# Kernel optimization log

Measured on AMD Instinct MI355X. Metric: run time of the kernel, lower is better.

## Reference

```python
import jax, jax.numpy as jnp
import numpy as np

IN_F, OUT_F, K = 1024, 1024, 12
EPS = 1e-6


def setup_inputs() -> dict:
    key = jax.random.key(0)
    k1, k2, k3, k4 = jax.random.split(key, 4)
    x = jax.random.normal(k1, (4, 4096, IN_F), dtype=jnp.float32)
    # grid: linspace(-2,2,K) per feature + small noise so sort is nontrivial
    base = jnp.linspace(-2.0, 2.0, K, dtype=jnp.float32)
    grid = base[None, :] + 0.1 * jax.random.normal(k2, (IN_F, K), dtype=jnp.float32)
    coeffs = 0.1 * jax.random.normal(k3, (IN_F, K), dtype=jnp.float32)
    tangents = jnp.zeros((IN_F, K), dtype=jnp.float32)
    knot_alive = jnp.full((IN_F, K), 3.0, dtype=jnp.float32)
    kw1, kw2 = jax.random.split(k4)
    proj_w = jax.random.normal(kw1, (OUT_F, IN_F), dtype=jnp.float32) / np.sqrt(IN_F)
    proj_b = jnp.zeros((OUT_F,), dtype=jnp.float32)
    res_w = jax.random.normal(kw2, (OUT_F, IN_F), dtype=jnp.float32) / np.sqrt(IN_F)
    return {"x": x, "grid": grid, "coeffs": coeffs, "tangents": tangents,
            "knot_alive": knot_alive, "proj_w": proj_w, "proj_b": proj_b, "res_w": res_w}


def _eval_hermite_spline(x, grid, coeffs, tangents, knot_alive):
    # sort knots per input feature (grid: [F,K])
    sort_idx = jnp.argsort(grid, axis=1)
    sorted_grid = jnp.take_along_axis(grid, sort_idx, axis=1)
    sorted_coeffs = jnp.take_along_axis(coeffs, sort_idx, axis=1)
    sorted_tangents = jnp.take_along_axis(tangents, sort_idx, axis=1)
    sorted_alive = jnp.take_along_axis(knot_alive, sort_idx, axis=1)
    alive = jax.nn.sigmoid(sorted_alive)
    mc = sorted_coeffs * alive          # masked heights [F,K]
    mt = sorted_tangents * alive        # masked tangents [F,K]

    orig_shape = x.shape
    xf = x.reshape(-1, orig_shape[-1])  # [M,F]
    gmin = sorted_grid[:, 0]            # [F]
    gmax = sorted_grid[:, -1]
    xc = jnp.clip(xf, gmin[None, :], gmax[None, :])
    grange = jnp.maximum(gmax - gmin, EPS)
    xn = (xc - gmin[None, :]) / grange[None, :] * (K - 1)  # [M,F]
    idx_l = jnp.clip(xn.astype(jnp.int32), 0, K - 2)
    t = xn - idx_l.astype(xf.dtype)

    feat = jnp.arange(xf.shape[1])[None, :]  # [1,F] broadcast against [M,F] idx
    p0 = mc[feat, idx_l]
    p1 = mc[feat, idx_l + 1]
    m0 = mt[feat, idx_l]
    m1 = mt[feat, idx_l + 1]
    x_left = sorted_grid[feat, idx_l]
    x_right = sorted_grid[feat, idx_l + 1]
    dx = jnp.maximum(x_right - x_left, EPS)

    t2 = t * t
    t3 = t2 * t
    h00 = 2 * t3 - 3 * t2 + 1
    h10 = t3 - 2 * t2 + t
    h01 = -2 * t3 + 3 * t2
    h11 = t3 - t2
    out = h00 * p0 + h10 * m0 * dx + h01 * p1 + h11 * m1 * dx
    return out.reshape(orig_shape)


def reference(x, grid, coeffs, tangents, knot_alive, proj_w, proj_b, res_w):
    spline_out = _eval_hermite_spline(x, grid, coeffs, tangents, knot_alive)
    # proj(spline_out) + residual(x); torch Linear: y = x @ W.T + b
    return (jnp.einsum('...i,oi->...o', spline_out, proj_w) + proj_b
            + jnp.einsum('...i,oi->...o', x, res_w))
```

## Files before the change

### kernel.cpp

```cpp
#include <hip/hip_runtime.h>
#include <hip/hip_bf16.h>


#define IN_F   1024
#define OUT_F  1024
#define KNOTS  12
#define M_ROWS 16384
#define GK     2048

#define BM   256
#define BN   256
#define BKT  32
#define NT   (GK / BKT)
#define NBUF 4

typedef __attribute__((ext_vector_type(8))) __bf16 bf16x8;
typedef __attribute__((ext_vector_type(4))) float  f32x4;

__device__ __forceinline__ unsigned short f2bf(float v) {
    unsigned int u = __float_as_uint(v);
    u = (u + 0x7fffu + ((u >> 16) & 1u)) >> 16;
    return (unsigned short)u;
}

__device__ __forceinline__ void gload16(const void* g, void* l) {
    __builtin_amdgcn_global_load_lds(
        (const __attribute__((address_space(1))) void*)g,
        (__attribute__((address_space(3))) void*)l, 16, 0, 0);
}

__global__ __launch_bounds__(256) void prep_kernel(
    const float* __restrict__ grid, const float* __restrict__ coeffs,
    const float* __restrict__ tangents, const float* __restrict__ alive,
    float* __restrict__ gmin, float* __restrict__ scale, float4* __restrict__ H)
{
    int f = blockIdx.x * blockDim.x + threadIdx.x;
    if (f >= IN_F) return;
    float g[KNOTS], c[KNOTS], t[KNOTS], a[KNOTS];
    for (int i = 0; i < KNOTS; ++i) {
        g[i] = grid[f*KNOTS+i];  c[i] = coeffs[f*KNOTS+i];
        t[i] = tangents[f*KNOTS+i]; a[i] = alive[f*KNOTS+i];
    }
    for (int i = 1; i < KNOTS; ++i) {
        float gk=g[i], ck=c[i], tk=t[i], ak=a[i];
        int j = i-1;
        while (j >= 0 && g[j] > gk) { g[j+1]=g[j]; c[j+1]=c[j]; t[j+1]=t[j]; a[j+1]=a[j]; --j; }
        g[j+1]=gk; c[j+1]=ck; t[j+1]=tk; a[j+1]=ak;
    }
    float mcl[KNOTS], mtl[KNOTS];
    for (int i = 0; i < KNOTS; ++i) {
        float s = 1.f / (1.f + expf(-a[i]));
        mcl[i] = c[i]*s;  mtl[i] = t[i]*s;
    }
    gmin[f] = g[0];
    float grange = fmaxf(g[KNOTS-1] - g[0], 1e-6f);
    scale[f] = (float)(KNOTS-1) / grange;
    for (int k = 0; k < KNOTS-1; ++k) {
        float dx = fmaxf(g[k+1]-g[k], 1e-6f);
        H[(size_t)f*KNOTS + k] = make_float4(mcl[k], mcl[k+1], mtl[k]*dx, mtl[k+1]*dx);
    }
    H[(size_t)f*KNOTS + KNOTS-1] = make_float4(0.f, 0.f, 0.f, 0.f);
}

#define SROWS 64
#define HPAD  13
__global__ __launch_bounds__(256) void spline_kernel(const float* __restrict__ x,
    const float* __restrict__ gmin, const float* __restrict__ scale,
    const float4* __restrict__ H, unsigned short* __restrict__ A)
{
    __shared__ float4 sH[256 * HPAD];
    const int tid = threadIdx.x;
    const int f   = blockIdx.y * 256 + tid;
    #pragma unroll
    for (int k = 0; k < KNOTS; ++k) sH[tid*HPAD + k] = H[(size_t)f*KNOTS + k];
    const float gm = gmin[f];
    const float sc = scale[f];
    __syncthreads();
    const int r0 = blockIdx.x * SROWS;
    #pragma unroll 4
    for (int r = 0; r < SROWS; ++r) {
        const int row = r0 + r;
        const float xi = x[(size_t)row*IN_F + f];
        float xn = (xi - gm) * sc;
        xn = fminf(fmaxf(xn, 0.f), (float)(KNOTS-1));
        int idx = (int)xn;  idx = idx > (KNOTS-2) ? (KNOTS-2) : idx;
        const float tt = xn - (float)idx;
        const float4 h = sH[tid*HPAD + idx];
        const float t2 = tt*tt, t3 = t2*tt;
        const float h00 =  2.f*t3 - 3.f*t2 + 1.f;
        const float h01 = -2.f*t3 + 3.f*t2;
        const float h10 =  t3 - 2.f*t2 + tt;
        const float h11 =  t3 - t2;
        const float sv  = h00*h.x + h01*h.y + h10*h.z + h11*h.w;
        const size_t base = (size_t)row * GK;
        A[base + f]        = f2bf(sv);
        A[base + IN_F + f] = f2bf(xi);
    }
}

__global__ __launch_bounds__(256) void bcast_kernel(
    const float* __restrict__ P, const float* __restrict__ R,
    unsigned short* __restrict__ Bc)
{
    int g = blockIdx.x*256 + threadIdx.x;
    int n  = g >> 9;
    int k4 = (g & 511) * 4;
    const float* src = (k4 < IN_F) ? (P + (size_t)n*IN_F + k4)
                                   : (R + (size_t)n*IN_F + (k4 - IN_F));
    float4 v = *reinterpret_cast<const float4*>(src);
    ushort4 o;
    o.x = f2bf(v.x); o.y = f2bf(v.y); o.z = f2bf(v.z); o.w = f2bf(v.w);
    *reinterpret_cast<ushort4*>(Bc + (size_t)n*GK + k4) = o;
}

__global__ __launch_bounds__(512, 2) void gemm_kernel(
    const unsigned short* __restrict__ A, const unsigned short* __restrict__ B,
    const float* __restrict__ bias, float* __restrict__ C)
{
    __shared__ unsigned short sA[NBUF][BM*BKT];
    __shared__ unsigned short sB[NBUF][BN*BKT];

    const int tid  = threadIdx.x;
    const int wg   = blockIdx.x;
    const int swz  = (wg & 7) * 32 + (wg >> 3);
    const int by   = swz >> 2;
    const int bx   = swz & 3;

    const int lane = tid & 63;
    const int wave = tid >> 6;
    const int wr   = wave >> 2;
    const int wc   = wave & 3;
    const int lr   = lane & 15;
    const int bsel = lane >> 4;

    const size_t aBase = (size_t)by * BM * GK;
    const size_t bBase = (size_t)bx * BN * GK;

    f32x4 acc[8][4] = {};

    auto stageA = [&](int t, int buf) {
        const int k0 = t * BKT;
        #pragma unroll
        for (int i = 0; i < 2; ++i) {
            const int L = i*512 + tid;
            const int row = L >> 2, c = L & 3;
            const int cs = c ^ ((row >> 1) & 3);
            gload16(A + aBase + (size_t)row*GK + k0 + cs*8, &sA[buf][(size_t)L*8]);
        }
    };
    auto stageB = [&](int t, int buf) {
        const int k0 = t * BKT;
        #pragma unroll
        for (int i = 0; i < 2; ++i) {
            const int L = i*512 + tid;
            const int row = L >> 2, c = L & 3;
            const int cs = c ^ ((row >> 1) & 3);
            gload16(B + bBase + (size_t)row*GK + k0 + cs*8, &sB[buf][(size_t)L*8]);
        }
    };
    auto ldA = [&](int buf, int row) -> bf16x8 {
        const int cs = bsel ^ ((row >> 1) & 3);
        return *reinterpret_cast<const bf16x8*>(&sA[buf][row*BKT + cs*8]);
    };
    auto ldB = [&](int buf, int row) -> bf16x8 {
        const int cs = bsel ^ ((row >> 1) & 3);
        return *reinterpret_cast<const bf16x8*>(&sB[buf][row*BKT + cs*8]);
    };

    stageA(0,0); stageB(0,0);
    stageA(1,1); stageB(1,1);
    stageA(2,2); stageB(2,2);

    for (int t = 0; t < NT; ++t) {
        const int buf = t & 3;
        if (t < NT-2)        asm volatile("s_waitcnt vmcnt(8)" ::: "memory");
        else if (t == NT-2)  asm volatile("s_waitcnt vmcnt(4)" ::: "memory");
        else                 asm volatile("s_waitcnt vmcnt(0)" ::: "memory");
        __builtin_amdgcn_s_barrier();

        bf16x8 a0[4], bfr[4];
        #pragma unroll
        for (int m = 0; m < 4; ++m) a0[m] = ldA(buf, wr*128 + m*16 + lr);
        #pragma unroll
        for (int n = 0; n < 4; ++n) bfr[n] = ldB(buf, wc*64 + n*16 + lr);
        if (t + 3 < NT) stageA(t+3, (t+3) & 3);
        __builtin_amdgcn_sched_barrier(0);
        __builtin_amdgcn_s_barrier();

        __builtin_amdgcn_s_setprio(1);
        #pragma unroll
        for (int m = 0; m < 4; ++m)
            #pragma unroll
            for (int n = 0; n < 4; ++n)
                acc[m][n] = __builtin_amdgcn_mfma_f32_16x16x32_bf16(a0[m], bfr[n], acc[m][n], 0, 0, 0);
        __builtin_amdgcn_s_setprio(0);

        bf16x8 a1[4];
        #pragma unroll
        for (int m = 0; m < 4; ++m) a1[m] = ldA(buf, wr*128 + 64 + m*16 + lr);
        if (t + 3 < NT) stageB(t+3, (t+3) & 3);
        __builtin_amdgcn_sched_barrier(0);
        __builtin_amdgcn_s_barrier();

        __builtin_amdgcn_s_setprio(1);
        #pragma unroll
        for (int m = 0; m < 4; ++m)
            #pragma unroll
            for (int n = 0; n < 4; ++n)
                acc[4+m][n] = __builtin_amdgcn_mfma_f32_16x16x32_bf16(a1[m], bfr[n], acc[4+m][n], 0, 0, 0);
        __builtin_amdgcn_s_setprio(0);
    }

    const int r0 = (lane >> 4) * 4;
    #pragma unroll
    for (int n = 0; n < 4; ++n) {
        const int col = bx*BN + wc*64 + n*16 + lr;
        const float bv = bias[col];
        #pragma unroll
        for (int m = 0; m < 8; ++m) {
            const int grow = by*BM + wr*128 + m*16 + r0;
            #pragma unroll
            for (int r = 0; r < 4; ++r)
                C[(size_t)(grow + r)*OUT_F + col] = acc[m][n][r] + bv;
        }
    }
}

__global__ __launch_bounds__(256) void fallback_kernel(
    const float* __restrict__ x, const float* __restrict__ P,
    const float* __restrict__ R, const float* __restrict__ pb,
    const float* __restrict__ gmin, const float* __restrict__ scale,
    const float4* __restrict__ H, float* __restrict__ out)
{
    __shared__ float s_s[IN_F];
    __shared__ float s_x[IN_F];
    int row = blockIdx.x;
    const float* xr = x + (size_t)row*IN_F;
    for (int f = threadIdx.x; f < IN_F; f += 256) {
        float xi = xr[f];
        float xn = (xi - gmin[f]) * scale[f];
        xn = fminf(fmaxf(xn, 0.f), (float)(KNOTS-1));
        int idx = (int)xn;  idx = idx > (KNOTS-2) ? (KNOTS-2) : idx;
        float tt = xn - (float)idx;
        float4 h = H[(size_t)f*KNOTS + idx];
        float t2 = tt*tt, t3 = t2*tt;
        s_s[f] = (2.f*t3-3.f*t2+1.f)*h.x + (-2.f*t3+3.f*t2)*h.y
               + (t3-2.f*t2+tt)*h.z + (t3-t2)*h.w;
        s_x[f] = xi;
    }
    __syncthreads();
    for (int j = 0; j < 4; ++j) {
        int o = threadIdx.x + j*256;
        const float* Pr = P + (size_t)o*IN_F;
        const float* Rr = R + (size_t)o*IN_F;
        float acc = pb[o];
        for (int f = 0; f < IN_F; ++f)
            acc = fmaf(s_s[f], Pr[f], fmaf(s_x[f], Rr[f], acc));
        out[(size_t)row*OUT_F + o] = acc;
    }
}

extern "C" void kernel_launch(void* const* d_in, const int* in_sizes, int n_in,
                              void* d_out, int out_size, void* d_ws, size_t ws_size,
                              hipStream_t stream) {
    const float* x         = (const float*)d_in[0];
    const float* grid      = (const float*)d_in[1];
    const float* coeffs    = (const float*)d_in[2];
    const float* tangents  = (const float*)d_in[3];
    const float* knotalive = (const float*)d_in[4];
    const float* proj_w    = (const float*)d_in[5];
    const float* proj_b    = (const float*)d_in[6];
    const float* res_w     = (const float*)d_in[7];
    float* out = (float*)d_out;

    const size_t needB  = (size_t)OUT_F * GK * 2;
    const size_t needA  = (size_t)M_ROWS * GK * 2;
    const size_t needT  = ((size_t)IN_F*2 + (size_t)IN_F*KNOTS*4) * 4;

    char* ws = (char*)d_ws;
    if (ws_size >= needB + needA + needT) {
        unsigned short* Bcat = (unsigned short*)ws;
        unsigned short* Abuf = (unsigned short*)(ws + needB);
        float*  gmin = (float*)(ws + needB + needA);
        float*  scl  = gmin + IN_F;
        float4* H    = (float4*)(scl + IN_F);

        prep_kernel<<<(IN_F+255)/256, 256, 0, stream>>>(grid, coeffs, tangents, knotalive,
                                                        gmin, scl, H);
        bcast_kernel<<<(OUT_F*GK/4)/256, 256, 0, stream>>>(proj_w, res_w, Bcat);
        spline_kernel<<<dim3(M_ROWS/SROWS, IN_F/256), 256, 0, stream>>>(x, gmin, scl, H, Abuf);
        gemm_kernel<<<(M_ROWS/BM)*(OUT_F/BN), 512, 0, stream>>>(Abuf, Bcat, proj_b, out);
    } else {
        float*  gmin = (float*)ws;
        float*  scl  = gmin + IN_F;
        float4* H    = (float4*)(scl + IN_F);
        prep_kernel<<<(IN_F+255)/256, 256, 0, stream>>>(grid, coeffs, tangents, knotalive,
                                                        gmin, scl, H);
        fallback_kernel<<<M_ROWS, 256, 0, stream>>>(x, proj_w, res_w, proj_b,
                                                    gmin, scl, H, out);
    }
}
```

Before: 112.1 us.

## Vectorize spline kernel over four features and trim GEMM loop barriers

```diff
diff --git a/kernel.cpp b/kernel.cpp
--- a/kernel.cpp
+++ b/kernel.cpp
@@ -62,39 +62,44 @@
     H[(size_t)f*KNOTS + KNOTS-1] = make_float4(0.f, 0.f, 0.f, 0.f);
 }
 
-#define SROWS 64
-#define HPAD  13
+#define SPB 32
 __global__ __launch_bounds__(256) void spline_kernel(const float* __restrict__ x,
     const float* __restrict__ gmin, const float* __restrict__ scale,
     const float4* __restrict__ H, unsigned short* __restrict__ A)
 {
-    __shared__ float4 sH[256 * HPAD];
     const int tid = threadIdx.x;
-    const int f   = blockIdx.y * 256 + tid;
-    #pragma unroll
-    for (int k = 0; k < KNOTS; ++k) sH[tid*HPAD + k] = H[(size_t)f*KNOTS + k];
-    const float gm = gmin[f];
-    const float sc = scale[f];
-    __syncthreads();
-    const int r0 = blockIdx.x * SROWS;
-    #pragma unroll 4
-    for (int r = 0; r < SROWS; ++r) {
+    const int f0  = tid * 4;
+    const float4 gm4 = *reinterpret_cast<const float4*>(gmin + f0);
+    const float4 sc4 = *reinterpret_cast<const float4*>(scale + f0);
+    const float gms[4] = {gm4.x, gm4.y, gm4.z, gm4.w};
+    const float scs[4] = {sc4.x, sc4.y, sc4.z, sc4.w};
+    const int r0 = blockIdx.x * SPB;
+    for (int r = 0; r < SPB; ++r) {
         const int row = r0 + r;
-        const float xi = x[(size_t)row*IN_F + f];
-        float xn = (xi - gm) * sc;
-        xn = fminf(fmaxf(xn, 0.f), (float)(KNOTS-1));
-        int idx = (int)xn;  idx = idx > (KNOTS-2) ? (KNOTS-2) : idx;
-        const float tt = xn - (float)idx;
-        const float4 h = sH[tid*HPAD + idx];
-        const float t2 = tt*tt, t3 = t2*tt;
-        const float h00 =  2.f*t3 - 3.f*t2 + 1.f;
-        const float h01 = -2.f*t3 + 3.f*t2;
-        const float h10 =  t3 - 2.f*t2 + tt;
-        const float h11 =  t3 - t2;
-        const float sv  = h00*h.x + h01*h.y + h10*h.z + h11*h.w;
+        const float4 xv = *reinterpret_cast<const float4*>(x + (size_t)row*IN_F + f0);
+        const float xs[4] = {xv.x, xv.y, xv.z, xv.w};
+        ushort4 so, xo;
+        unsigned short* sp = (unsigned short*)&so;
+        unsigned short* xp = (unsigned short*)&xo;
+        #pragma unroll
+        for (int j = 0; j < 4; ++j) {
+            const float xi = xs[j];
+            float xn = (xi - gms[j]) * scs[j];
+            xn = fminf(fmaxf(xn, 0.f), (float)(KNOTS-1));
+            int idx = (int)xn;  idx = idx > (KNOTS-2) ? (KNOTS-2) : idx;
+            const float tt = xn - (float)idx;
+            const float4 h = H[(size_t)(f0+j)*KNOTS + idx];
+            const float t2 = tt*tt, t3 = t2*tt;
+            const float h00 =  2.f*t3 - 3.f*t2 + 1.f;
+            const float h01 = -2.f*t3 + 3.f*t2;
+            const float h10 =  t3 - 2.f*t2 + tt;
+            const float h11 =  t3 - t2;
+            sp[j] = f2bf(h00*h.x + h01*h.y + h10*h.z + h11*h.w);
+            xp[j] = f2bf(xi);
+        }
         const size_t base = (size_t)row * GK;
-        A[base + f]        = f2bf(sv);
-        A[base + IN_F + f] = f2bf(xi);
+        *reinterpret_cast<ushort4*>(A + base + f0)        = so;
+        *reinterpret_cast<ushort4*>(A + base + IN_F + f0) = xo;
     }
 }
 
@@ -184,8 +189,6 @@
         #pragma unroll
         for (int n = 0; n < 4; ++n) bfr[n] = ldB(buf, wc*64 + n*16 + lr);
         if (t + 3 < NT) stageA(t+3, (t+3) & 3);
-        __builtin_amdgcn_sched_barrier(0);
-        __builtin_amdgcn_s_barrier();
 
         __builtin_amdgcn_s_setprio(1);
         #pragma unroll
@@ -194,13 +197,12 @@
             for (int n = 0; n < 4; ++n)
                 acc[m][n] = __builtin_amdgcn_mfma_f32_16x16x32_bf16(a0[m], bfr[n], acc[m][n], 0, 0, 0);
         __builtin_amdgcn_s_setprio(0);
+        __builtin_amdgcn_s_barrier();
 
         bf16x8 a1[4];
         #pragma unroll
         for (int m = 0; m < 4; ++m) a1[m] = ldA(buf, wr*128 + 64 + m*16 + lr);
         if (t + 3 < NT) stageB(t+3, (t+3) & 3);
-        __builtin_amdgcn_sched_barrier(0);
-        __builtin_amdgcn_s_barrier();
 
         __builtin_amdgcn_s_setprio(1);
         #pragma unroll
@@ -288,7 +290,7 @@
         prep_kernel<<<(IN_F+255)/256, 256, 0, stream>>>(grid, coeffs, tangents, knotalive,
                                                         gmin, scl, H);
         bcast_kernel<<<(OUT_F*GK/4)/256, 256, 0, stream>>>(proj_w, res_w, Bcat);
-        spline_kernel<<<dim3(M_ROWS/SROWS, IN_F/256), 256, 0, stream>>>(x, gmin, scl, H, Abuf);
+        spline_kernel<<<M_ROWS/SPB, 256, 0, stream>>>(x, gmin, scl, H, Abuf);
         gemm_kernel<<<(M_ROWS/BM)*(OUT_F/BN), 512, 0, stream>>>(Abuf, Bcat, proj_b, out);
     } else {
         float*  gmin = (float*)ws;
```

Result: slower. 155.2 us (+38.4%).
